# Kernel tuning notes

Hardware: AMD Instinct MI355X
Metric: run time of the kernel (lower is better)

## Reference

```python
import jax, jax.numpy as jnp
import numpy as np

D_MODEL, D_STATE, D_CONV, EXPAND = 1024, 16, 4, 2
D_INNER = EXPAND * D_MODEL
B, L = 2, 2048
DT = 0.1  # module hard-codes dt = 0.1 (dt_proj is unused)


def setup_inputs() -> dict:
    key = jax.random.key(0)
    ks = jax.random.split(key, 7)
    s = 0.02
    x = jax.random.normal(ks[0], (B, L, D_MODEL), dtype=jnp.float32)
    in_proj_w = jax.random.normal(ks[1], (2 * D_INNER, D_MODEL), dtype=jnp.float32) * s
    conv_w = jax.random.normal(ks[2], (D_INNER, 1, D_CONV), dtype=jnp.float32) * s
    conv_b = jnp.zeros((D_INNER,), dtype=jnp.float32)
    x_proj_w = jax.random.normal(ks[3], (2 * D_STATE, D_INNER), dtype=jnp.float32) * s
    A_log = jnp.log(jnp.tile(jnp.arange(1, D_STATE + 1, dtype=jnp.float32), (D_INNER, 1)))
    D_param = jnp.ones((D_INNER,), dtype=jnp.float32)
    out_proj_w = jax.random.normal(ks[4], (D_MODEL, D_INNER), dtype=jnp.float32) * s
    return {"x": x, "in_proj_w": in_proj_w, "conv_w": conv_w, "conv_b": conv_b,
            "x_proj_w": x_proj_w, "A_log": A_log, "D_param": D_param,
            "out_proj_w": out_proj_w}


def _silu(v):
    return v * jax.nn.sigmoid(v)


def reference(x, in_proj_w, conv_w, conv_b, x_proj_w, A_log, D_param, out_proj_w):
    # in_proj: (B,L,d_model) -> (B,L,2*d_inner)
    xz = jnp.einsum('bld,ed->ble', x, in_proj_w)
    xs, z = jnp.split(xz, 2, axis=-1)
    # depthwise causal conv1d (torch pads both sides d_conv-1 then slices [:L] == left-pad only)
    xc = jax.lax.conv_general_dilated(
        xs.transpose(0, 2, 1), conv_w, window_strides=(1,),
        padding=[(D_CONV - 1, 0)], dimension_numbers=('NCH', 'OIH', 'NCH'),
        feature_group_count=D_INNER) + conv_b[None, :, None]
    xs = _silu(xc.transpose(0, 2, 1))  # (B, L, d_inner)
    # x_proj -> B_proj, C_proj  (B,L,d_state) each
    x_dbl = jnp.einsum('bld,ed->ble', xs, x_proj_w)
    B_proj, C_proj = jnp.split(x_dbl, 2, axis=-1)
    # SSM scan; dt is constant 0.1 so dA = exp(dt*A) is time-invariant
    A = -jnp.exp(A_log)                 # (d_inner, d_state)
    dA = jnp.exp(DT * A)                # (d_inner, d_state)

    def step(h, inp):
        x_t, B_t, C_t = inp             # (B,D), (B,N), (B,N)
        h = dA[None] * h + DT * B_t[:, None, :] * x_t[:, :, None]
        y_t = jnp.einsum('bdn,bn->bd', h, C_t)
        return h, y_t

    h0 = jnp.zeros((B, D_INNER, D_STATE), dtype=xs.dtype)
    _, ys = jax.lax.scan(step, h0,
                         (xs.transpose(1, 0, 2), B_proj.transpose(1, 0, 2), C_proj.transpose(1, 0, 2)))
    y = ys.transpose(1, 0, 2) + xs * D_param[None, None, :]
    y = y * _silu(z)
    return jnp.einsum('bld,ed->ble', y, out_proj_w)
```

## Files before the change

### kernel.cpp

```cpp
#include <hip/hip_runtime.h>
#include <hip/hip_bf16.h>
#include <math.h>

#define D_MODEL 1024
#define D_STATE 16
#define D_CONV  4
#define D_INNER 2048
#define BATCH   2
#define SEQ     2048
#define M_TOTAL (BATCH*SEQ)
#define DT_VAL  0.1f

#define CHUNK 64
#define WARM  32
#define NCHUNK (SEQ / CHUNK)
#define TSTEP 8

typedef __attribute__((ext_vector_type(8))) __bf16 bf16x8;
typedef __attribute__((ext_vector_type(4))) __bf16 bf16x4;
typedef __attribute__((ext_vector_type(4))) float floatx4;

__device__ __forceinline__ void gld_lds16(const __bf16* g, __bf16* l) {
    __builtin_amdgcn_global_load_lds(
        (const __attribute__((address_space(1))) void*)g,
        (__attribute__((address_space(3))) void*)l, 16, 0, 0);
}

__global__ __launch_bounds__(512, 4) void inproj_v9(
    const __bf16* __restrict__ A, const __bf16* __restrict__ W,
    __bf16* __restrict__ O1, __bf16* __restrict__ O2)
{
    __shared__ __bf16 As[2][256][32];
    __shared__ __bf16 Bs[2][128][32];
    constexpr int LDA = 1024;

    const int tid = threadIdx.x;
    const int bid = blockIdx.x;
    const int r8  = bid & 7;
    const int i   = bid >> 3;
    const int mt  = (r8 & 3) * 4 + (i & 3);
    const int nt  = (r8 >> 2) * 16 + (i >> 2);
    const int m0  = mt * 256;
    const int n0  = nt * 128;

    const int wave = tid >> 6;
    const int lane = tid & 63;
    const int wr   = (wave >> 1) << 6;
    const int wc   = (wave & 1) << 6;
    const int fm   = lane & 15;
    const int coff = (((lane >> 4) ^ ((fm >> 1) & 3)) << 3);

    const int srow = tid >> 2;
    const int sc   = tid & 3;
    const int sgc  = sc ^ ((srow >> 1) & 3);
    const __bf16* ga = A + (size_t)(m0 + srow) * LDA + sgc * 8;
    const __bf16* gb = W + (size_t)(n0 + srow) * LDA + sgc * 8;
    const size_t rstep = (size_t)128 * LDA;
    __bf16* la = &As[0][srow][sc * 8];
    __bf16* lb = &Bs[0][srow][sc * 8];

    floatx4 acc[4][4];
    #pragma unroll
    for (int a = 0; a < 4; ++a)
        #pragma unroll
        for (int b = 0; b < 4; ++b)
            acc[a][b] = (floatx4){0.f, 0.f, 0.f, 0.f};

    for (int k0 = 0; k0 < 1024; k0 += 64) {
        __syncthreads();
        #pragma unroll
        for (int p = 0; p < 2; ++p) {
            gld_lds16(ga + k0 + p * 32,         la + p * 8192);
            gld_lds16(ga + k0 + p * 32 + rstep, la + p * 8192 + 4096);
            gld_lds16(gb + k0 + p * 32,         lb + p * 4096);
        }
        __syncthreads();

        #pragma unroll
        for (int p = 0; p < 2; ++p) {
            bf16x8 af[4], bf[4];
            #pragma unroll
            for (int a = 0; a < 4; ++a)
                af[a] = *(const bf16x8*)(&As[p][wr + a * 16 + fm][0] + coff);
            #pragma unroll
            for (int b = 0; b < 4; ++b)
                bf[b] = *(const bf16x8*)(&Bs[p][wc + b * 16 + fm][0] + coff);
            #pragma unroll
            for (int a = 0; a < 4; ++a)
                #pragma unroll
                for (int b = 0; b < 4; ++b)
                    acc[a][b] = __builtin_amdgcn_mfma_f32_16x16x32_bf16(
                        af[a], bf[b], acc[a][b], 0, 0, 0);
        }
    }

    const int crow = (lane >> 4) << 2;
    const int ccol = lane & 15;
    #pragma unroll
    for (int a = 0; a < 4; ++a) {
        #pragma unroll
        for (int b = 0; b < 4; ++b) {
            const int cm = m0 + wr + a * 16 + crow;
            const int cn = n0 + wc + b * 16 + ccol;
            #pragma unroll
            for (int r = 0; r < 4; ++r) {
                const float v = acc[a][b][r];
                if (n0 < 2048) {
                    O1[(size_t)(cm + r) * 2048 + cn] = (__bf16)v;
                } else {
                    const float s = v / (1.f + __expf(-v));
                    O2[(size_t)(cm + r) * 2048 + cn - 2048] = (__bf16)s;
                }
            }
        }
    }
}

__global__ __launch_bounds__(256) void outproj_gemm(
    const __bf16* __restrict__ A, const __bf16* __restrict__ W,
    float* __restrict__ out)
{
    __shared__ __bf16 As[2][128][32];
    __shared__ __bf16 Bs[2][64][32];

    const int tid  = threadIdx.x;
    const int bid  = blockIdx.x;
    const int xcd  = bid & 7;
    const int i    = bid >> 3;
    const int byl  = i & 3;
    const int bx   = i >> 2;
    const int m0   = (xcd * 4 + byl) * 128;
    const int n0   = bx * 64;

    const int wave = tid >> 6;
    const int lane = tid & 63;
    const int wr   = (wave >> 1) << 6;
    const int wc   = (wave & 1) << 5;
    const int fm   = lane & 15;
    const int coff = (((lane >> 4) ^ ((fm >> 1) & 3)) << 3);
    const int grow = lane >> 2;
    const int sgc8 = (((lane & 3) ^ ((grow >> 1) & 3)) << 3);
    const int arow = wave * 16 + grow;
    const int ldst = (lane & 3) << 3;

    floatx4 acc[4][2];
    #pragma unroll
    for (int a = 0; a < 4; ++a)
        #pragma unroll
        for (int b = 0; b < 2; ++b)
            acc[a][b] = (floatx4){0.f, 0.f, 0.f, 0.f};

    const __bf16* ap = A + (size_t)(m0 + arow) * 2048 + sgc8;
    const __bf16* wp = W + (size_t)(n0 + arow) * 2048 + sgc8;

    for (int k0 = 0; k0 < 2048; k0 += 64) {
        __syncthreads();
        #pragma unroll
        for (int p = 0; p < 2; ++p) {
            gld_lds16(ap + k0 + p * 32,                     &As[p][arow][ldst]);
            gld_lds16(ap + k0 + p * 32 + (size_t)64 * 2048, &As[p][arow + 64][ldst]);
            gld_lds16(wp + k0 + p * 32,                     &Bs[p][arow][ldst]);
        }
        __syncthreads();

        #pragma unroll
        for (int p = 0; p < 2; ++p) {
            bf16x8 af[4], bfv[2];
            #pragma unroll
            for (int a = 0; a < 4; ++a)
                af[a] = *(const bf16x8*)(&As[p][wr + a * 16 + fm][0] + coff);
            #pragma unroll
            for (int b = 0; b < 2; ++b)
                bfv[b] = *(const bf16x8*)(&Bs[p][wc + b * 16 + fm][0] + coff);
            #pragma unroll
            for (int a = 0; a < 4; ++a)
                #pragma unroll
                for (int b = 0; b < 2; ++b)
                    acc[a][b] = __builtin_amdgcn_mfma_f32_16x16x32_bf16(
                        af[a], bfv[b], acc[a][b], 0, 0, 0);
        }
    }

    const int crow = (lane >> 4) << 2;
    const int ccol = lane & 15;
    #pragma unroll
    for (int a = 0; a < 4; ++a) {
        #pragma unroll
        for (int b = 0; b < 2; ++b) {
            const int cm = m0 + wr + a * 16 + crow;
            const int cn = n0 + wc + b * 16 + ccol;
            #pragma unroll
            for (int r = 0; r < 4; ++r)
                out[(size_t)(cm + r) * D_MODEL + cn] = acc[a][b][r];
        }
    }
}

__global__ __launch_bounds__(256) void xproj_conv(
    const __bf16* __restrict__ xsp, const float* __restrict__ cw,
    const float* __restrict__ cb, const __bf16* __restrict__ Wp,
    float* __restrict__ bc, __bf16* __restrict__ xsc)
{
    __shared__ __bf16 Wsh[32][264];

    const int tid  = threadIdx.x;
    const int bid  = blockIdx.x;
    const int ks   = bid & 7;
    const int mb   = bid >> 3;
    const int m0   = mb * 128;
    const int koff = ks * 256;
    const int wave = tid >> 6;
    const int lane = tid & 63;
    const int fm   = lane & 15;
    const int fk   = (lane >> 4) << 3;
    const bool boundary = (m0 & (SEQ - 1)) == 0;

    {
        const int r = tid >> 3;
        const int c = (tid & 7) << 5;
        #pragma unroll
        for (int q = 0; q < 4; ++q)
            *(bf16x8*)&Wsh[r][c + q * 8] =
                *(const bf16x8*)(Wp + (size_t)r * D_INNER + koff + c + q * 8);
    }
    __syncthreads();

    floatx4 acc[2][2];
    #pragma unroll
    for (int a = 0; a < 2; ++a)
        #pragma unroll
        for (int b = 0; b < 2; ++b)
            acc[a][b] = (floatx4){0.f, 0.f, 0.f, 0.f};

    const int r1 = wave * 32 + fm;

    for (int kit = 0; kit < 8; ++kit) {
        const int kg = koff + kit * 32;
        const int dc = kg + fk;

        float w0[8], w1[8], w2[8], w3[8], bv[8];
        #pragma unroll
        for (int c = 0; c < 8; ++c) {
            const float4 wq = *(const float4*)(cw + (size_t)(dc + c) * 4);
            w0[c] = wq.x; w1[c] = wq.y; w2[c] = wq.z; w3[c] = wq.w;
            bv[c] = cb[dc + c];
        }

        bf16x8 af[2];
        #pragma unroll
        for (int a = 0; a < 2; ++a) {
            const int rr = r1 + a * 16;
            float o[8];
            #pragma unroll
            for (int c = 0; c < 8; ++c) o[c] = bv[c];
            #pragma unroll
            for (int j = 0; j < 4; ++j) {
                const int tr = rr - 3 + j;
                float tap[8];
                if (!boundary || tr >= 0) {
                    const bf16x8 tv = *(const bf16x8*)(
                        xsp + (size_t)(m0 + tr) * D_INNER + dc);
                    #pragma unroll
                    for (int c = 0; c < 8; ++c) tap[c] = (float)tv[c];
                } else {
                    #pragma unroll
                    for (int c = 0; c < 8; ++c) tap[c] = 0.f;
                }
                #pragma unroll
                for (int c = 0; c < 8; ++c) {
                    const float wj = (j==0)?w0[c]:(j==1)?w1[c]:(j==2)?w2[c]:w3[c];
                    o[c] = fmaf(wj, tap[c], o[c]);
                }
            }
            #pragma unroll
            for (int c = 0; c < 8; ++c)
                o[c] = o[c] / (1.f + __expf(-o[c]));
            bf16x8 ob;
            #pragma unroll
            for (int c = 0; c < 8; ++c) ob[c] = (__bf16)o[c];
            af[a] = ob;
            *(bf16x8*)(xsc + (size_t)(m0 + rr) * D_INNER + dc) = ob;
        }

        bf16x8 wf[2];
        wf[0] = *(bf16x8*)&Wsh[fm][kit * 32 + fk];
        wf[1] = *(bf16x8*)&Wsh[16 + fm][kit * 32 + fk];
        #pragma unroll
        for (int a = 0; a < 2; ++a)
            #pragma unroll
            for (int b = 0; b < 2; ++b)
                acc[a][b] = __builtin_amdgcn_mfma_f32_16x16x32_bf16(
                    af[a], wf[b], acc[a][b], 0, 0, 0);
    }

    const int crow = (lane >> 4) << 2;
    const int ccol = lane & 15;
    #pragma unroll
    for (int a = 0; a < 2; ++a)
        #pragma unroll
        for (int b = 0; b < 2; ++b)
            #pragma unroll
            for (int r = 0; r < 4; ++r)
                atomicAdd(bc + (size_t)(m0 + wave * 32 + a * 16 + crow + r) * 32
                             + b * 16 + ccol, acc[a][b][r]);
}

__global__ __launch_bounds__(256) void cast5(
    const float* __restrict__ x, const float* __restrict__ win,
    const float* __restrict__ wout, const float* __restrict__ xpw,
    __bf16* __restrict__ xbf, __bf16* __restrict__ winbf,
    __bf16* __restrict__ woutbf, __bf16* __restrict__ xpwbf,
    float* __restrict__ bcz)
{
    const size_t g = (size_t)(blockIdx.x * 256 + threadIdx.x);
    if (g >= 2637824) {
        const size_t off = (g - 2637824) * 4;
        *(float4*)(bcz + off) = (float4){0.f, 0.f, 0.f, 0.f};
        return;
    }
    const size_t j = g * 4;
    const float* src; __bf16* dst; size_t off;
    if (j < 4194304)       { src = x;    dst = xbf;    off = j; }
    else if (j < 8388608)  { src = win;  dst = winbf;  off = j - 4194304; }
    else if (j < 10485760) { src = wout; dst = woutbf; off = j - 8388608; }
    else                   { src = xpw;  dst = xpwbf;  off = j - 10485760; }
    const float4 v = *(const float4*)(src + off);
    bf16x4 o;
    o[0] = (__bf16)v.x; o[1] = (__bf16)v.y; o[2] = (__bf16)v.z; o[3] = (__bf16)v.w;
    *(bf16x4*)(dst + off) = o;
}

__global__ __launch_bounds__(256) void ssm_scan(
    const __bf16* __restrict__ xsc, const float* __restrict__ bc,
    const __bf16* __restrict__ szbf, __bf16* __restrict__ ybf,
    const float* __restrict__ alog, const float* __restrict__ dpar)
{
    __shared__ float Bsh[CHUNK + WARM][16];
    __shared__ float Csh[CHUNK + WARM][16];
    __shared__ float Xsh[2][TSTEP][256];
    __shared__ float Zsh[2][TSTEP][256];

    const int tid = threadIdx.x;
    const int blk = blockIdx.x;
    const int db  = blk & 7;
    const int ch  = (blk >> 3) & (NCHUNK - 1);
    const int b   = blk >> 8;
    const int d0  = db * 256;
    const int d   = d0 + tid;
    const int t0  = ch * CHUNK;
    const int tw  = (t0 >= WARM) ? (t0 - WARM) : 0;
    const int warm = t0 - tw;
    const int nt  = t0 + CHUNK - tw;
    const int ntiles = nt / TSTEP;

    const float* bcp = bc + ((size_t)b * SEQ + tw) * 32;
    for (int i = tid; i < nt * 8; i += 256) {
        const int row = i >> 3, q = i & 7;
        const float4 v = *(const float4*)(bcp + (size_t)row * 32 + q * 4);
        if (q < 4) *(float4*)&Bsh[row][q * 4] = v;
        else       *(float4*)&Csh[row][(q - 4) * 4] = v;
    }

    float dAv[16], h[16];
    #pragma unroll
    for (int q = 0; q < 4; ++q) {
        const float4 av = *(const float4*)(alog + (size_t)d * D_STATE + q * 4);
        dAv[q*4+0] = expf(-DT_VAL * expf(av.x));
        dAv[q*4+1] = expf(-DT_VAL * expf(av.y));
        dAv[q*4+2] = expf(-DT_VAL * expf(av.z));
        dAv[q*4+3] = expf(-DT_VAL * expf(av.w));
    }
    #pragma unroll
    for (int n = 0; n < 16; ++n) h[n] = 0.f;
    const float Dd = dpar[d];

    const __bf16* xbase = xsc  + ((size_t)b * SEQ + tw) * D_INNER + d0;
    const __bf16* zbase = szbf + ((size_t)b * SEQ + tw) * D_INNER + d0;
    __bf16*       ybase = ybf  + ((size_t)b * SEQ + tw) * D_INNER + d0;

    const int lrow = tid >> 6;
    const int lcol = (tid & 63) << 2;

    {
        const bf16x4 xa = *(const bf16x4*)(xbase + (size_t)lrow * D_INNER + lcol);
        const bf16x4 xb = *(const bf16x4*)(xbase + (size_t)(lrow + 4) * D_INNER + lcol);
        float4 fa, fb;
        fa.x=(float)xa[0]; fa.y=(float)xa[1]; fa.z=(float)xa[2]; fa.w=(float)xa[3];
        fb.x=(float)xb[0]; fb.y=(float)xb[1]; fb.z=(float)xb[2]; fb.w=(float)xb[3];
        *(float4*)&Xsh[0][lrow][lcol]     = fa;
        *(float4*)&Xsh[0][lrow + 4][lcol] = fb;
        if (warm == 0) {
            const bf16x4 za = *(const bf16x4*)(zbase + (size_t)lrow * D_INNER + lcol);
            const bf16x4 zb = *(const bf16x4*)(zbase + (size_t)(lrow + 4) * D_INNER + lcol);
            float4 ga, gb;
            ga.x=(float)za[0]; ga.y=(float)za[1]; ga.z=(float)za[2]; ga.w=(float)za[3];
            gb.x=(float)zb[0]; gb.y=(float)zb[1]; gb.z=(float)zb[2]; gb.w=(float)zb[3];
            *(float4*)&Zsh[0][lrow][lcol]     = ga;
            *(float4*)&Zsh[0][lrow + 4][lcol] = gb;
        }
    }
    __syncthreads();

    for (int tile = 0; tile < ntiles; ++tile) {
        const int buf = tile & 1;
        const int s   = tile * TSTEP;
        const int s2  = s + TSTEP;
        const bool more = (tile + 1 < ntiles);
        const bool znext = more && (s2 >= warm);

        bf16x4 rx0, rx1, rz0, rz1;
        if (more) {
            rx0 = *(const bf16x4*)(xbase + (size_t)(s2 + lrow) * D_INNER + lcol);
            rx1 = *(const bf16x4*)(xbase + (size_t)(s2 + lrow + 4) * D_INNER + lcol);
        }
        if (znext) {
            rz0 = *(const bf16x4*)(zbase + (size_t)(s2 + lrow) * D_INNER + lcol);
            rz1 = *(const bf16x4*)(zbase + (size_t)(s2 + lrow + 4) * D_INNER + lcol);
        }

        #pragma unroll
        for (int tt = 0; tt < TSTEP; ++tt) {
            const int t = s + tt;
            const float x   = Xsh[buf][tt][tid];
            const float dtx = DT_VAL * x;
            float y0 = 0.f, y1 = 0.f, y2 = 0.f, y3 = 0.f;
            #pragma unroll
            for (int n = 0; n < 4; ++n) {
                h[n]      = fmaf(dAv[n],      h[n],      dtx * Bsh[t][n]);
                h[n + 4]  = fmaf(dAv[n + 4],  h[n + 4],  dtx * Bsh[t][n + 4]);
                h[n + 8]  = fmaf(dAv[n + 8],  h[n + 8],  dtx * Bsh[t][n + 8]);
                h[n + 12] = fmaf(dAv[n + 12], h[n + 12], dtx * Bsh[t][n + 12]);
                y0 = fmaf(h[n],      Csh[t][n],      y0);
                y1 = fmaf(h[n + 4],  Csh[t][n + 4],  y1);
                y2 = fmaf(h[n + 8],  Csh[t][n + 8],  y2);
                y3 = fmaf(h[n + 12], Csh[t][n + 12], y3);
            }
            if (t >= warm) {
                const float sz = Zsh[buf][tt][tid];
                const float y  = fmaf(x, Dd, (y0 + y1) + (y2 + y3));
                ybase[(size_t)t * D_INNER + tid] = (__bf16)(y * sz);
            }
        }

        if (more) {
            float4 fa, fb;
            fa.x=(float)rx0[0]; fa.y=(float)rx0[1]; fa.z=(float)rx0[2]; fa.w=(float)rx0[3];
            fb.x=(float)rx1[0]; fb.y=(float)rx1[1]; fb.z=(float)rx1[2]; fb.w=(float)rx1[3];
            *(float4*)&Xsh[buf ^ 1][lrow][lcol]     = fa;
            *(float4*)&Xsh[buf ^ 1][lrow + 4][lcol] = fb;
        }
        if (znext) {
            float4 ga, gb;
            ga.x=(float)rz0[0]; ga.y=(float)rz0[1]; ga.z=(float)rz0[2]; ga.w=(float)rz0[3];
            gb.x=(float)rz1[0]; gb.y=(float)rz1[1]; gb.z=(float)rz1[2]; gb.w=(float)rz1[3];
            *(float4*)&Zsh[buf ^ 1][lrow][lcol]     = ga;
            *(float4*)&Zsh[buf ^ 1][lrow + 4][lcol] = gb;
        }
        __syncthreads();
    }
}

extern "C" void kernel_launch(void* const* d_in, const int* in_sizes, int n_in,
                              void* d_out, int out_size, void* d_ws, size_t ws_size,
                              hipStream_t stream)
{
    const float* x    = (const float*)d_in[0];
    const float* win  = (const float*)d_in[1];
    const float* cw   = (const float*)d_in[2];
    const float* cb   = (const float*)d_in[3];
    const float* xpw  = (const float*)d_in[4];
    const float* alog = (const float*)d_in[5];
    const float* dpar = (const float*)d_in[6];
    const float* wout = (const float*)d_in[7];
    float* out = (float*)d_out;

    char* w = (char*)d_ws;
    __bf16* szbf   = (__bf16*)(w + 33554432);
    __bf16* xspbf  = (__bf16*)(w + 50331648);
    __bf16* xsc    = (__bf16*)(w + 67108864);
    float*  bcbuf  = (float*)(w + 83886080);
    __bf16* r1     = (__bf16*)(w + 84410368);
    __bf16* xbf    = r1;
    __bf16* winbf  = r1 + 4194304;
    __bf16* ybf    = r1;
    __bf16* woutbf = (__bf16*)(w + 101187584);
    __bf16* xpwbf  = (__bf16*)(w + 105381888);

    cast5<<<10432, 256, 0, stream>>>(x, win, wout, xpw,
                                     xbf, winbf, woutbf, xpwbf, bcbuf);
    inproj_v9<<<512, 512, 0, stream>>>(xbf, winbf, xspbf, szbf);
    xproj_conv<<<256, 256, 0, stream>>>(xspbf, cw, cb, xpwbf, bcbuf, xsc);
    ssm_scan<<<BATCH * NCHUNK * 8, 256, 0, stream>>>(
        xsc, bcbuf, szbf, ybf, alog, dpar);
    outproj_gemm<<<512, 256, 0, stream>>>(ybf, woutbf, out);
}
```

Measured before the change: 218.6 us.

## Rewrite in-projection GEMM with 256x256 tiles and double-buffered async LDS pipeline

The in-projection GEMM moves from 256x128 tiles with single-stage loads to 256x256 tiles, launching 256 blocks instead of 512. Global-to-LDS loads for the next k-steps are double-buffered and interleaved with MFMA quarters, using explicit waitcnt, barriers and setprio, so load latency overlaps compute. The larger tile raises arithmetic intensity per LDS byte, but it doubles the accumulators per wave, lowers occupancy to 2 blocks, and leaves only 256 blocks, which may underfill the CUs.

```diff
diff --git a/kernel.cpp b/kernel.cpp
--- a/kernel.cpp
+++ b/kernel.cpp
@@ -26,27 +26,28 @@
         (__attribute__((address_space(3))) void*)l, 16, 0, 0);
 }
 
-__global__ __launch_bounds__(512, 4) void inproj_v9(
+__global__ __launch_bounds__(512, 2) void inproj_8p(
     const __bf16* __restrict__ A, const __bf16* __restrict__ W,
     __bf16* __restrict__ O1, __bf16* __restrict__ O2)
 {
-    __shared__ __bf16 As[2][256][32];
-    __shared__ __bf16 Bs[2][128][32];
+    __shared__ __bf16 As[2][2][256][32];
+    __shared__ __bf16 Bs[2][2][256][32];
     constexpr int LDA = 1024;
+    constexpr int NT  = 16;
 
     const int tid = threadIdx.x;
     const int bid = blockIdx.x;
     const int r8  = bid & 7;
-    const int i   = bid >> 3;
-    const int mt  = (r8 & 3) * 4 + (i & 3);
-    const int nt  = (r8 >> 2) * 16 + (i >> 2);
+    const int w32 = bid >> 3;
+    const int mt  = (r8 & 3) * 4 + (w32 & 3);
+    const int nt  = (r8 >> 2) * 8 + (w32 >> 2);
     const int m0  = mt * 256;
-    const int n0  = nt * 128;
+    const int n0  = nt * 256;
 
     const int wave = tid >> 6;
     const int lane = tid & 63;
-    const int wr   = (wave >> 1) << 6;
-    const int wc   = (wave & 1) << 6;
+    const int wr   = (wave >> 2) * 128;
+    const int wc   = (wave & 3) * 64;
     const int fm   = lane & 15;
     const int coff = (((lane >> 4) ^ ((fm >> 1) & 3)) << 3);
 
@@ -56,48 +57,104 @@
     const __bf16* ga = A + (size_t)(m0 + srow) * LDA + sgc * 8;
     const __bf16* gb = W + (size_t)(n0 + srow) * LDA + sgc * 8;
     const size_t rstep = (size_t)128 * LDA;
-    __bf16* la = &As[0][srow][sc * 8];
-    __bf16* lb = &Bs[0][srow][sc * 8];
-
-    floatx4 acc[4][4];
-    #pragma unroll
-    for (int a = 0; a < 4; ++a)
+    __bf16* la = &As[0][0][srow][sc * 8];
+    __bf16* lb = &Bs[0][0][srow][sc * 8];
+
+    const __bf16* fa0 = &As[0][0][wr + fm][0] + coff;
+    const __bf16* fb0 = &Bs[0][0][wc + fm][0] + coff;
+
+    floatx4 acc[8][4];
+    #pragma unroll
+    for (int a = 0; a < 8; ++a)
         #pragma unroll
         for (int b = 0; b < 4; ++b)
             acc[a][b] = (floatx4){0.f, 0.f, 0.f, 0.f};
 
-    for (int k0 = 0; k0 < 1024; k0 += 64) {
-        __syncthreads();
-        #pragma unroll
-        for (int p = 0; p < 2; ++p) {
-            gld_lds16(ga + k0 + p * 32,         la + p * 8192);
-            gld_lds16(ga + k0 + p * 32 + rstep, la + p * 8192 + 4096);
-            gld_lds16(gb + k0 + p * 32,         lb + p * 4096);
-        }
-        __syncthreads();
-
-        #pragma unroll
-        for (int p = 0; p < 2; ++p) {
-            bf16x8 af[4], bf[4];
-            #pragma unroll
-            for (int a = 0; a < 4; ++a)
-                af[a] = *(const bf16x8*)(&As[p][wr + a * 16 + fm][0] + coff);
-            #pragma unroll
-            for (int b = 0; b < 4; ++b)
-                bf[b] = *(const bf16x8*)(&Bs[p][wc + b * 16 + fm][0] + coff);
-            #pragma unroll
-            for (int a = 0; a < 4; ++a)
-                #pragma unroll
-                for (int b = 0; b < 4; ++b)
-                    acc[a][b] = __builtin_amdgcn_mfma_f32_16x16x32_bf16(
-                        af[a], bf[b], acc[a][b], 0, 0, 0);
-        }
-    }
+#define STAGE_A(u, kp) {                                                       \
+        const int _d = (((u) & 1) << 14) + ((kp) << 13);                       \
+        const size_t _g = (size_t)(u) * 64 + (kp) * 32;                        \
+        gld_lds16(ga + _g,         la + _d);                                   \
+        gld_lds16(ga + _g + rstep, la + _d + 4096); }
+#define STAGE_B(u, kp) {                                                       \
+        const int _d = (((u) & 1) << 14) + ((kp) << 13);                       \
+        const size_t _g = (size_t)(u) * 64 + (kp) * 32;                        \
+        gld_lds16(gb + _g,         lb + _d);                                   \
+        gld_lds16(gb + _g + rstep, lb + _d + 4096); }
+#define STAGE_A_FULL(u) if ((u) < NT) { STAGE_A(u, 0); STAGE_A(u, 1); }
+#define STAGE_B_FULL(u) if ((u) < NT) { STAGE_B(u, 0); STAGE_B(u, 1); }
+
+#define LOADQ(q)                                                               \
+    _Pragma("unroll")                                                          \
+    for (int a2 = 0; a2 < 2; ++a2)                                             \
+        _Pragma("unroll")                                                      \
+        for (int ks = 0; ks < 2; ++ks)                                         \
+            afr[a2][ks] = *(const bf16x8*)(fA + ks * 8192 + ((q)*2 + a2) * 512);
+#define MFMAQ(q)                                                               \
+    __builtin_amdgcn_s_setprio(1);                                             \
+    _Pragma("unroll")                                                          \
+    for (int ks = 0; ks < 2; ++ks)                                             \
+        _Pragma("unroll")                                                      \
+        for (int a2 = 0; a2 < 2; ++a2)                                         \
+            _Pragma("unroll")                                                  \
+            for (int b = 0; b < 4; ++b)                                        \
+                acc[(q)*2 + a2][b] = __builtin_amdgcn_mfma_f32_16x16x32_bf16(  \
+                    afr[a2][ks], bfr[b][ks], acc[(q)*2 + a2][b], 0, 0, 0);     \
+    __builtin_amdgcn_s_setprio(0);
+
+    STAGE_A_FULL(0); STAGE_B_FULL(0);
+    STAGE_B_FULL(1); STAGE_A_FULL(1);
+    asm volatile("s_waitcnt vmcnt(8)" ::: "memory");
+    __builtin_amdgcn_s_barrier();
+
+    for (int t = 0; t < NT; ++t) {
+        const int s = t & 1;
+        const __bf16* fA = fa0 + (s << 14);
+        const __bf16* fB = fb0 + (s << 14);
+        bf16x8 bfr[4][2], afr[2][2];
+
+        #pragma unroll
+        for (int b = 0; b < 4; ++b)
+            #pragma unroll
+            for (int ks = 0; ks < 2; ++ks)
+                bfr[b][ks] = *(const bf16x8*)(fB + ks * 8192 + b * 512);
+        LOADQ(0);
+        asm volatile("s_waitcnt lgkmcnt(0)" ::: "memory");
+        __builtin_amdgcn_sched_barrier(0);
+        __builtin_amdgcn_s_barrier();
+        STAGE_B_FULL(t + 2);
+        asm volatile("" ::: "memory");
+        MFMAQ(0);
+
+        LOADQ(1);
+        MFMAQ(1);
+        LOADQ(2);
+        MFMAQ(2);
+
+        LOADQ(3);
+        asm volatile("s_waitcnt lgkmcnt(0)" ::: "memory");
+        __builtin_amdgcn_sched_barrier(0);
+        __builtin_amdgcn_s_barrier();
+        STAGE_A_FULL(t + 2);
+        asm volatile("" ::: "memory");
+        MFMAQ(3);
+        if (t < NT - 2) {
+            asm volatile("s_waitcnt vmcnt(8)" ::: "memory");
+        } else if (t == NT - 2) {
+            asm volatile("s_waitcnt vmcnt(0)" ::: "memory");
+        }
+        if (t < NT - 1) __builtin_amdgcn_s_barrier();
+    }
+#undef STAGE_A
+#undef STAGE_B
+#undef STAGE_A_FULL
+#undef STAGE_B_FULL
+#undef LOADQ
+#undef MFMAQ
 
     const int crow = (lane >> 4) << 2;
     const int ccol = lane & 15;
     #pragma unroll
-    for (int a = 0; a < 4; ++a) {
+    for (int a = 0; a < 8; ++a) {
         #pragma unroll
         for (int b = 0; b < 4; ++b) {
             const int cm = m0 + wr + a * 16 + crow;
@@ -108,8 +165,8 @@
                 if (n0 < 2048) {
                     O1[(size_t)(cm + r) * 2048 + cn] = (__bf16)v;
                 } else {
-                    const float s = v / (1.f + __expf(-v));
-                    O2[(size_t)(cm + r) * 2048 + cn - 2048] = (__bf16)s;
+                    const float sg = v / (1.f + __expf(-v));
+                    O2[(size_t)(cm + r) * 2048 + cn - 2048] = (__bf16)sg;
                 }
             }
         }
@@ -488,7 +545,7 @@
 
     cast5<<<10432, 256, 0, stream>>>(x, win, wout, xpw,
                                      xbf, winbf, woutbf, xpwbf, bcbuf);
-    inproj_v9<<<512, 512, 0, stream>>>(xbf, winbf, xspbf, szbf);
+    inproj_8p<<<256, 512, 0, stream>>>(xbf, winbf, xspbf, szbf);
     xproj_conv<<<256, 256, 0, stream>>>(xspbf, cw, cb, xpwbf, bcbuf, xsc);
     ssm_scan<<<BATCH * NCHUNK * 8, 256, 0, stream>>>(
         xsc, bcbuf, szbf, ybf, alog, dpar);
```

Measured after the change: 222.5 us. No clear change (+1.8%).
